# Kernel optimization log

Measured on AMD Instinct MI355X. Metric: run time of the kernel, lower is better.

Reference implementation:

```python
import jax, jax.numpy as jnp
import numpy as np

B, D, H, W = 32, 256, 32, 32
K = 1024
COMMITMENT_COST = 0.25


def setup_inputs() -> dict:
    key = jax.random.key(0)
    k1, k2 = jax.random.split(key)
    z = jax.random.normal(k1, (B, D, H, W), dtype=jnp.float32)
    # torch init: uniform_(-1/K, 1/K)
    emb_weight = jax.random.uniform(k2, (K, D), dtype=jnp.float32,
                                    minval=-1.0 / K, maxval=1.0 / K)
    return {"z": z, "emb_weight": emb_weight}


def reference(z, emb_weight):
    b, c, h, w = z.shape
    # [B, D, H, W] -> [B*H*W, D]
    z_flat = jnp.transpose(z, (0, 2, 3, 1)).reshape(-1, c)
    # squared-distance: ||z||^2 + ||e||^2 - 2 z.e  -> [N, K]
    distances = (jnp.sum(z_flat ** 2, axis=1, keepdims=True)
                 + jnp.sum(emb_weight ** 2, axis=1)[None, :]
                 - 2.0 * jnp.matmul(z_flat, emb_weight.T))
    encoding_indices = jnp.argmin(distances, axis=1)  # [N]
    z_q = emb_weight[encoding_indices]                # [N, D]
    z_q = z_q.reshape(b, h, w, c).transpose(0, 3, 1, 2)  # [B, D, H, W]

    q_latent_loss = jnp.mean((jax.lax.stop_gradient(z_q) - z) ** 2)
    e_latent_loss = jnp.mean((z_q - jax.lax.stop_gradient(z)) ** 2)
    loss = q_latent_loss + COMMITMENT_COST * e_latent_loss

    # straight-through estimator
    z_q = z + jax.lax.stop_gradient(z_q - z)
    return z_q, loss, encoding_indices
```

## Files before the change

kernel.cpp:

```cpp
#include <hip/hip_runtime.h>

#define NPTS  32768
#define DIM   256

#define ZQ_OFF   0
#define LOSS_OFF 8388608
#define IDX_OFF  8388609

typedef __attribute__((ext_vector_type(8))) short short8;
typedef __attribute__((ext_vector_type(4))) float f32x4;
typedef unsigned short ushort_t;
typedef unsigned int u32;
typedef unsigned long long u64;

__device__ __forceinline__ int z_base(int n) { return ((n >> 10) << 18) | (n & 1023); }

__device__ __forceinline__ ushort_t f2bf(float f) {
    u32 u = __float_as_uint(f);
    u += 0x7FFFu + ((u >> 16) & 1u);
    return (ushort_t)(u >> 16);
}

__device__ __forceinline__ u64 pack_vi(float v, int i) {
    u32 u = __float_as_uint(v);
    u32 key = (u & 0x80000000u) ? ~u : u;
    return ((u64)key << 32) | (u32)i;
}

__device__ __forceinline__ float np_half_sq(const float* __restrict__ p, int stride) {
    float S[16];
#pragma unroll
    for (int l = 0; l < 16; ++l) {
        float t[8];
#pragma unroll
        for (int j = 0; j < 8; ++j) {
            float v = p[(j * 16 + l) * stride];
            t[j] = __fmul_rn(v, v);
        }
        S[l] = __fadd_rn(__fadd_rn(__fadd_rn(t[0], t[1]), __fadd_rn(t[2], t[3])),
                         __fadd_rn(__fadd_rn(t[4], t[5]), __fadd_rn(t[6], t[7])));
    }
    float u[8];
#pragma unroll
    for (int i = 0; i < 8; ++i) u[i] = __fadd_rn(S[i], S[i + 8]);
    float v4[4];
#pragma unroll
    for (int i = 0; i < 4; ++i) v4[i] = __fadd_rn(u[i], u[i + 4]);
    return __fadd_rn(__fadd_rn(v4[0], v4[2]), __fadd_rn(v4[1], v4[3]));
}
__device__ __forceinline__ float np_sum256_sq(const float* __restrict__ p, int stride) {
    return __fadd_rn(np_half_sq(p, stride), np_half_sq(p + 128 * stride, stride));
}

__device__ __forceinline__ float np_half_sq_abs(const float* __restrict__ p, int stride, float* aacc) {
    float S[16]; float a = *aacc;
#pragma unroll
    for (int l = 0; l < 16; ++l) {
        float t[8];
#pragma unroll
        for (int j = 0; j < 8; ++j) {
            float v = p[(j * 16 + l) * stride];
            t[j] = __fmul_rn(v, v);
            a = __fadd_rn(a, fabsf(v));
        }
        S[l] = __fadd_rn(__fadd_rn(__fadd_rn(t[0], t[1]), __fadd_rn(t[2], t[3])),
                         __fadd_rn(__fadd_rn(t[4], t[5]), __fadd_rn(t[6], t[7])));
    }
    float u[8];
#pragma unroll
    for (int i = 0; i < 8; ++i) u[i] = __fadd_rn(S[i], S[i + 8]);
    float v4[4];
#pragma unroll
    for (int i = 0; i < 4; ++i) v4[i] = __fadd_rn(u[i], u[i + 4]);
    *aacc = a;
    return __fadd_rn(__fadd_rn(v4[0], v4[2]), __fadd_rn(v4[1], v4[3]));
}

__global__ __launch_bounds__(256) void setup_kernel(
    const float* __restrict__ z, const float* __restrict__ emb,
    float* __restrict__ z2, float* __restrict__ eps,
    float* __restrict__ e2, float* __restrict__ e2h,
    ushort_t* __restrict__ ebf, u64* __restrict__ bestG,
    double* __restrict__ loss_acc, unsigned int* __restrict__ ticket)
{
    if (blockIdx.x < 128) {
        int n = blockIdx.x * 256 + threadIdx.x;
        const float* p = z + z_base(n);
        float a = 0.0f;
        float h0 = np_half_sq_abs(p, 1024, &a);
        float h1 = np_half_sq_abs(p + 128 * 1024, 1024, &a);
        z2[n] = __fadd_rn(h0, h1);
        eps[n] = __builtin_fmaf(1e-5f, a, 3e-4f);
        bestG[n] = 0x7FFFFFFFFFFFFFFFULL;
        if (blockIdx.x == 0 && threadIdx.x == 0) { *loss_acc = 0.0; *ticket = 0u; }
    } else {
        int kb = (blockIdx.x - 128) * 64;
        for (int i = threadIdx.x; i < 2048; i += 256) {
            int klocal = i >> 5, c = i & 31;
            int k = kb + klocal;
            int dt = c >> 2, lq = c & 3;
            int kt = k >> 5, nt = (k >> 4) & 1, lr = k & 15;
            const float* e = emb + k * 256 + dt * 32 + lq * 8;
            short8 ov;
#pragma unroll
            for (int j = 0; j < 8; ++j) ov[j] = (short)f2bf(e[j]);
            int f = kt * 16 + nt * 8 + dt;
            *(short8*)(ebf + (f << 9) + ((lq << 4) + lr) * 8) = ov;
        }
        if (threadIdx.x < 64) {
            int k = kb + threadIdx.x;
            float s = np_sum256_sq(emb + k * DIM, 1);
            e2[k] = s;
            e2h[k] = 0.5f * s;
        }
    }
}

__global__ __launch_bounds__(256, 4) void dist_kernel(
    const float* __restrict__ z, const float* __restrict__ emb,
    const ushort_t* __restrict__ ebf,
    const float* __restrict__ z2w, const float* __restrict__ e2w,
    const float* __restrict__ e2hw, const float* __restrict__ epsw,
    u64* __restrict__ bestG)
{
    __shared__ __align__(16) float zx[32 * 68];
    __shared__ __align__(16) int cl[2048];
    __shared__ float e2hS[1024];
    __shared__ unsigned int cntS[64];
    __shared__ int ovfS;

    const int tid = threadIdx.x;
    const int w  = tid >> 6;
    const int l  = tid & 63;
    const int lq = l >> 4;
    const int lr = l & 15;
    const int n0 = blockIdx.x << 6;
    const int zb = z_base(n0);
    const int pbase = w << 4;

    if (tid < 64) cntS[tid] = 0u;
    if (tid == 0) ovfS = 0;
    for (int i = tid; i < 1024; i += 256) e2hS[i] = e2hw[i];

    short8 af[8];
    {
        const float* zp = z + zb + pbase + lr;
#pragma unroll
        for (int dt = 0; dt < 8; ++dt)
#pragma unroll
            for (int j = 0; j < 8; ++j)
                af[dt][j] = (short)f2bf(zp[((dt << 5) + (lq << 3) + j) << 10]);
    }

    float4 epsv = *(const float4*)(epsw + n0 + pbase + (lq << 2));
    float eps_r[4] = { epsv.x, epsv.y, epsv.z, epsv.w };
    float Mr[4] = { -3.4e38f, -3.4e38f, -3.4e38f, -3.4e38f };

    __syncthreads();

    const ushort_t* fb = ebf + (l << 3);
    short8 B[2][2];
    B[0][0] = *(const short8*)(fb + (0 << 9));
    B[0][1] = *(const short8*)(fb + (8 << 9));
    B[1][0] = *(const short8*)(fb + (1 << 9));
    B[1][1] = *(const short8*)(fb + (9 << 9));

    f32x4 acc[2];
#pragma unroll
    for (int nt = 0; nt < 2; ++nt) {
        float e = e2hS[(nt << 4) + lr];
        f32x4 iv = { -e, -e, -e, -e };
        acc[nt] = iv;
    }

#pragma unroll 1
    for (int kt = 0; kt < 32; ++kt) {
        const int kt1 = (kt < 31) ? kt + 1 : 0;
#pragma unroll
        for (int dt = 0; dt < 8; ++dt) {
            const int p = dt & 1;
            __builtin_amdgcn_s_setprio(1);
            acc[0] = __builtin_amdgcn_mfma_f32_16x16x32_bf16(af[dt], B[p][0], acc[0], 0, 0, 0);
            acc[1] = __builtin_amdgcn_mfma_f32_16x16x32_bf16(af[dt], B[p][1], acc[1], 0, 0, 0);
            __builtin_amdgcn_s_setprio(0);
            const int dtn = dt + 2;
            const int fk = (dtn < 8) ? kt : kt1;
            const int f0 = fk * 16 + (dtn & 7);
            B[p][0] = *(const short8*)(fb + (f0 << 9));
            B[p][1] = *(const short8*)(fb + ((f0 + 8) << 9));
        }
        {
            float mx[4], thr[4];
#pragma unroll
            for (int r = 0; r < 4; ++r) mx[r] = fmaxf(acc[0][r], acc[1][r]);
#pragma unroll
            for (int s = 1; s <= 8; s <<= 1)
#pragma unroll
                for (int r = 0; r < 4; ++r)
                    mx[r] = fmaxf(mx[r], __shfl_xor(mx[r], s, 64));
#pragma unroll
            for (int r = 0; r < 4; ++r) {
                Mr[r] = fmaxf(Mr[r], mx[r]);
                thr[r] = Mr[r] - eps_r[r];
            }
#pragma unroll
            for (int nt = 0; nt < 2; ++nt)
#pragma unroll
                for (int r = 0; r < 4; ++r) {
                    if (acc[nt][r] >= thr[r]) {
                        int pp = pbase + lq * 4 + r;
                        int kk = (kt << 5) + (nt << 4) + lr;
                        unsigned int pos = atomicAdd(&cntS[pp], 1u);
                        if (pos < 32u) cl[pp * 32 + pos] = kk;
                        else atomicMax(&ovfS, 1);
                    }
                }
        }
        if (kt < 31) {
#pragma unroll
            for (int nt = 0; nt < 2; ++nt) {
                float e = e2hS[(kt1 << 5) + (nt << 4) + lr];
                f32x4 iv = { -e, -e, -e, -e };
                acc[nt] = iv;
            }
        }
    }
    __syncthreads();

    const int pt = tid & 63;
    const int s0 = tid >> 6;
    unsigned int nc = cntS[pt]; if (nc > 32u) nc = 32u;
    bool  act[8]; int kE[8]; float accE[8];
#pragma unroll
    for (int j = 0; j < 8; ++j) {
        unsigned int s = (unsigned int)s0 + 4u * j;
        act[j] = s < nc;
        kE[j] = act[j] ? cl[pt * 32 + s] : 0;
        accE[j] = 0.0f;
    }
#pragma unroll 1
    for (int dt = 0; dt < 8; ++dt) {
        const int dbase = dt * 32;
        __syncthreads();
        {
            int q = tid & 15, dd0 = tid >> 4;
            float4 v0 = *(const float4*)(z + zb + ((dbase + dd0) << 10) + 4 * q);
            float4 v1 = *(const float4*)(z + zb + ((dbase + dd0 + 16) << 10) + 4 * q);
            *(float4*)(zx + dd0 * 68 + 4 * q) = v0;
            *(float4*)(zx + (dd0 + 16) * 68 + 4 * q) = v1;
        }
        __syncthreads();
#pragma unroll
        for (int j = 0; j < 8; ++j) {
            if (!act[j]) continue;
            const float* er = emb + kE[j] * 256 + dbase;
            float ev[32];
#pragma unroll
            for (int c = 0; c < 8; ++c) *(float4*)(ev + 4 * c) = *(const float4*)(er + 4 * c);
            float a = accE[j];
#pragma unroll
            for (int dd = 0; dd < 32; ++dd)
                a = __builtin_fmaf(zx[dd * 68 + pt], ev[dd], a);
            accE[j] = a;
        }
    }
#pragma unroll
    for (int j = 0; j < 8; ++j) {
        if (!act[j]) continue;
        int k = kE[j];
        float t1 = __fadd_rn(z2w[n0 + pt], e2w[k]);
        float d  = __fsub_rn(t1, __fmul_rn(2.0f, accE[j]));
        atomicMin(&bestG[n0 + pt], pack_vi(d, k));
    }
    __syncthreads();

    if (ovfS) {
        for (int row = 0; row < 64; ++row) {
            if (cntS[row] <= 32u) continue;
            float fa[4] = {0.f, 0.f, 0.f, 0.f};
            for (int dt = 0; dt < 8; ++dt) {
                const int dbase = dt * 32;
                __syncthreads();
                {
                    int q = tid & 15, dd0 = tid >> 4;
                    float4 v0 = *(const float4*)(z + zb + ((dbase + dd0) << 10) + 4 * q);
                    float4 v1 = *(const float4*)(z + zb + ((dbase + dd0 + 16) << 10) + 4 * q);
                    *(float4*)(zx + dd0 * 68 + 4 * q) = v0;
                    *(float4*)(zx + (dd0 + 16) * 68 + 4 * q) = v1;
                }
                __syncthreads();
                for (int c = 0; c < 4; ++c) {
                    const float* er = emb + (tid + 256 * c) * 256 + dbase;
                    for (int dd = 0; dd < 32; ++dd)
                        fa[c] = __builtin_fmaf(zx[dd * 68 + row], er[dd], fa[c]);
                }
            }
            for (int c = 0; c < 4; ++c) {
                int k = tid + 256 * c;
                float t1 = __fadd_rn(z2w[n0 + row], e2w[k]);
                float d  = __fsub_rn(t1, __fmul_rn(2.0f, fa[c]));
                atomicMin(&bestG[n0 + row], pack_vi(d, k));
            }
            __syncthreads();
        }
    }
}

__global__ __launch_bounds__(256) void zq_loss_kernel(
    const float* __restrict__ z, const float* __restrict__ emb,
    const u64* __restrict__ bestG, float* __restrict__ zq,
    double* __restrict__ loss_acc, unsigned int* __restrict__ ticket,
    float* __restrict__ out_loss, float* __restrict__ out_idx)
{
    const int tl = threadIdx.x & 63;
    const int q  = threadIdx.x >> 6;
    const int n  = blockIdx.x * 64 + tl;
    const int kk = (int)(u32)(bestG[n] & 0xFFFFFFFFULL);
    if (q == 0) out_idx[n] = (float)kk;
    const float4* er4 = (const float4*)(emb + kk * DIM + (q << 6));
    const int zb2 = z_base(n) + (q << 16);
    double s = 0.0;
#pragma unroll 4
    for (int c = 0; c < 16; ++c) {
        float4 e4 = er4[c];
#pragma unroll
        for (int j = 0; j < 4; ++j) {
            int dd = c * 4 + j;
            float ev = (j == 0) ? e4.x : (j == 1) ? e4.y : (j == 2) ? e4.z : e4.w;
            float zv = z[zb2 + (dd << 10)];
            zq[zb2 + (dd << 10)] = ev;
            float df = ev - zv;
            s = fma((double)df, (double)df, s);
        }
    }
    for (int off = 32; off; off >>= 1) s += __shfl_down(s, off, 64);
    __shared__ double sred[4];
    if ((threadIdx.x & 63) == 0) sred[threadIdx.x >> 6] = s;
    __syncthreads();
    if (threadIdx.x == 0) {
        atomicAdd(loss_acc, (sred[0] + sred[1]) + (sred[2] + sred[3]));
        __threadfence();
        unsigned int old = atomicAdd(ticket, 1u);
        if (old == gridDim.x - 1) {
            double total = atomicAdd(loss_acc, 0.0);
            out_loss[0] = (float)(1.25 * (total / 8388608.0));
        }
    }
}

extern "C" void kernel_launch(void* const* d_in, const int* in_sizes, int n_in,
                              void* d_out, int out_size, void* d_ws, size_t ws_size,
                              hipStream_t stream) {
    const float* z   = (const float*)d_in[0];
    const float* emb = (const float*)d_in[1];
    float* out = (float*)d_out;

    float* z2w = (float*)d_ws;
    float* epsw = (float*)((char*)d_ws + 131072);
    float* e2w = (float*)((char*)d_ws + 262144);
    float* e2hw = (float*)((char*)d_ws + 266240);
    ushort_t* ebf = (ushort_t*)((char*)d_ws + 270336);
    double* loss_acc = (double*)((char*)d_ws + 794624);
    unsigned int* ticket = (unsigned int*)((char*)d_ws + 794632);
    u64* bestG = (u64*)((char*)d_ws + 794640);

    setup_kernel<<<144, 256, 0, stream>>>(z, emb, z2w, epsw, e2w, e2hw, ebf,
                                          bestG, loss_acc, ticket);
    dist_kernel<<<NPTS / 64, 256, 0, stream>>>(z, emb, ebf, z2w, e2w, e2hw,
                                               epsw, bestG);
    zq_loss_kernel<<<NPTS / 64, 256, 0, stream>>>(z, emb, bestG, out + ZQ_OFF,
                                                  loss_acc, ticket,
                                                  out + LOSS_OFF, out + IDX_OFF);
}
```

Before: 218.1 us.

## Retile distance kernel to 2x2 MFMA tiles and split setup/zq work finer

```diff
diff --git a/kernel.cpp b/kernel.cpp
--- a/kernel.cpp
+++ b/kernel.cpp
@@ -83,18 +83,23 @@
     ushort_t* __restrict__ ebf, u64* __restrict__ bestG,
     double* __restrict__ loss_acc, unsigned int* __restrict__ ticket)
 {
-    if (blockIdx.x < 128) {
-        int n = blockIdx.x * 256 + threadIdx.x;
-        const float* p = z + z_base(n);
+    if (blockIdx.x < 256) {
+        __shared__ float hbuf[128], abuf[128];
+        const int tl = threadIdx.x & 127;
+        const int half = threadIdx.x >> 7;
+        const int n = blockIdx.x * 128 + tl;
+        const float* p = z + z_base(n) + (half << 17);
         float a = 0.0f;
-        float h0 = np_half_sq_abs(p, 1024, &a);
-        float h1 = np_half_sq_abs(p + 128 * 1024, 1024, &a);
-        z2[n] = __fadd_rn(h0, h1);
-        eps[n] = __builtin_fmaf(1e-5f, a, 3e-4f);
-        bestG[n] = 0x7FFFFFFFFFFFFFFFULL;
+        float hs = np_half_sq_abs(p, 1024, &a);
+        if (half) { hbuf[tl] = hs; abuf[tl] = a; bestG[n] = 0x7FFFFFFFFFFFFFFFULL; }
+        __syncthreads();
+        if (!half) {
+            z2[n] = __fadd_rn(hs, hbuf[tl]);
+            eps[n] = __builtin_fmaf(1e-5f, a + abuf[tl], 3e-4f);
+        }
         if (blockIdx.x == 0 && threadIdx.x == 0) { *loss_acc = 0.0; *ticket = 0u; }
     } else {
-        int kb = (blockIdx.x - 128) * 64;
+        int kb = (blockIdx.x - 256) * 64;
         for (int i = threadIdx.x; i < 2048; i += 256) {
             int klocal = i >> 5, c = i & 31;
             int k = kb + klocal;
@@ -116,7 +121,7 @@
     }
 }
 
-__global__ __launch_bounds__(256, 4) void dist_kernel(
+__global__ __launch_bounds__(256, 2) void dist_kernel(
     const float* __restrict__ z, const float* __restrict__ emb,
     const ushort_t* __restrict__ ebf,
     const float* __restrict__ z2w, const float* __restrict__ e2w,
@@ -131,97 +136,119 @@
 
     const int tid = threadIdx.x;
     const int w  = tid >> 6;
+    const int ph = w & 1;
+    const int kh = w >> 1;
     const int l  = tid & 63;
     const int lq = l >> 4;
     const int lr = l & 15;
     const int n0 = blockIdx.x << 6;
     const int zb = z_base(n0);
-    const int pbase = w << 4;
+    const int pbase = ph << 5;
 
     if (tid < 64) cntS[tid] = 0u;
     if (tid == 0) ovfS = 0;
     for (int i = tid; i < 1024; i += 256) e2hS[i] = e2hw[i];
 
-    short8 af[8];
-    {
-        const float* zp = z + zb + pbase + lr;
+    short8 af[2][8];
+#pragma unroll
+    for (int mt = 0; mt < 2; ++mt) {
+        const float* zp = z + zb + pbase + (mt << 4) + lr;
 #pragma unroll
         for (int dt = 0; dt < 8; ++dt)
 #pragma unroll
             for (int j = 0; j < 8; ++j)
-                af[dt][j] = (short)f2bf(zp[((dt << 5) + (lq << 3) + j) << 10]);
-    }
-
-    float4 epsv = *(const float4*)(epsw + n0 + pbase + (lq << 2));
-    float eps_r[4] = { epsv.x, epsv.y, epsv.z, epsv.w };
-    float Mr[4] = { -3.4e38f, -3.4e38f, -3.4e38f, -3.4e38f };
+                af[mt][dt][j] = (short)f2bf(zp[((dt << 5) + (lq << 3) + j) << 10]);
+    }
+
+    float eps_r[2][4], Mr[2][4];
+#pragma unroll
+    for (int mt = 0; mt < 2; ++mt) {
+        float4 ev = *(const float4*)(epsw + n0 + pbase + (mt << 4) + (lq << 2));
+        eps_r[mt][0] = ev.x; eps_r[mt][1] = ev.y; eps_r[mt][2] = ev.z; eps_r[mt][3] = ev.w;
+#pragma unroll
+        for (int r = 0; r < 4; ++r) Mr[mt][r] = -3.4e38f;
+    }
 
     __syncthreads();
 
     const ushort_t* fb = ebf + (l << 3);
-    short8 B[2][2];
-    B[0][0] = *(const short8*)(fb + (0 << 9));
-    B[0][1] = *(const short8*)(fb + (8 << 9));
-    B[1][0] = *(const short8*)(fb + (1 << 9));
-    B[1][1] = *(const short8*)(fb + (9 << 9));
-
-    f32x4 acc[2];
+    const int ktg0 = kh << 4;
+    short8 B[4][2];
+#pragma unroll
+    for (int i = 0; i < 4; ++i) {
+        const int f0 = (ktg0 << 4) + i;
+        B[i][0] = *(const short8*)(fb + (f0 << 9));
+        B[i][1] = *(const short8*)(fb + ((f0 + 8) << 9));
+    }
+
+    f32x4 acc[2][2];
 #pragma unroll
     for (int nt = 0; nt < 2; ++nt) {
-        float e = e2hS[(nt << 4) + lr];
+        float e = e2hS[(ktg0 << 5) + (nt << 4) + lr];
         f32x4 iv = { -e, -e, -e, -e };
-        acc[nt] = iv;
+        acc[0][nt] = iv; acc[1][nt] = iv;
     }
 
 #pragma unroll 1
-    for (int kt = 0; kt < 32; ++kt) {
-        const int kt1 = (kt < 31) ? kt + 1 : 0;
+    for (int kt = 0; kt < 16; ++kt) {
+        const int ktg = ktg0 + kt;
 #pragma unroll
         for (int dt = 0; dt < 8; ++dt) {
-            const int p = dt & 1;
+            const int p = dt & 3;
             __builtin_amdgcn_s_setprio(1);
-            acc[0] = __builtin_amdgcn_mfma_f32_16x16x32_bf16(af[dt], B[p][0], acc[0], 0, 0, 0);
-            acc[1] = __builtin_amdgcn_mfma_f32_16x16x32_bf16(af[dt], B[p][1], acc[1], 0, 0, 0);
+            acc[0][0] = __builtin_amdgcn_mfma_f32_16x16x32_bf16(af[0][dt], B[p][0], acc[0][0], 0, 0, 0);
+            acc[0][1] = __builtin_amdgcn_mfma_f32_16x16x32_bf16(af[0][dt], B[p][1], acc[0][1], 0, 0, 0);
+            acc[1][0] = __builtin_amdgcn_mfma_f32_16x16x32_bf16(af[1][dt], B[p][0], acc[1][0], 0, 0, 0);
+            acc[1][1] = __builtin_amdgcn_mfma_f32_16x16x32_bf16(af[1][dt], B[p][1], acc[1][1], 0, 0, 0);
             __builtin_amdgcn_s_setprio(0);
-            const int dtn = dt + 2;
-            const int fk = (dtn < 8) ? kt : kt1;
-            const int f0 = fk * 16 + (dtn & 7);
-            B[p][0] = *(const short8*)(fb + (f0 << 9));
-            B[p][1] = *(const short8*)(fb + ((f0 + 8) << 9));
+            const int ndt = (dt + 4) & 7;
+            const int nktg = (dt >= 4) ? ((ktg + 1) & 31) : ktg;
+            const int nf0 = (nktg << 4) + ndt;
+            B[p][0] = *(const short8*)(fb + (nf0 << 9));
+            B[p][1] = *(const short8*)(fb + ((nf0 + 8) << 9));
         }
         {
-            float mx[4], thr[4];
-#pragma unroll
-            for (int r = 0; r < 4; ++r) mx[r] = fmaxf(acc[0][r], acc[1][r]);
+            float mx[2][4], thr[2][4];
+#pragma unroll
+            for (int mt = 0; mt < 2; ++mt)
+#pragma unroll
+                for (int r = 0; r < 4; ++r)
+                    mx[mt][r] = fmaxf(acc[mt][0][r], acc[mt][1][r]);
 #pragma unroll
             for (int s = 1; s <= 8; s <<= 1)
 #pragma unroll
-                for (int r = 0; r < 4; ++r)
-                    mx[r] = fmaxf(mx[r], __shfl_xor(mx[r], s, 64));
-#pragma unroll
-            for (int r = 0; r < 4; ++r) {
-                Mr[r] = fmaxf(Mr[r], mx[r]);
-                thr[r] = Mr[r] - eps_r[r];
-            }
-#pragma unroll
-            for (int nt = 0; nt < 2; ++nt)
+                for (int mt = 0; mt < 2; ++mt)
+#pragma unroll
+                    for (int r = 0; r < 4; ++r)
+                        mx[mt][r] = fmaxf(mx[mt][r], __shfl_xor(mx[mt][r], s, 64));
+#pragma unroll
+            for (int mt = 0; mt < 2; ++mt)
 #pragma unroll
                 for (int r = 0; r < 4; ++r) {
-                    if (acc[nt][r] >= thr[r]) {
-                        int pp = pbase + lq * 4 + r;
-                        int kk = (kt << 5) + (nt << 4) + lr;
-                        unsigned int pos = atomicAdd(&cntS[pp], 1u);
-                        if (pos < 32u) cl[pp * 32 + pos] = kk;
-                        else atomicMax(&ovfS, 1);
+                    Mr[mt][r] = fmaxf(Mr[mt][r], mx[mt][r]);
+                    thr[mt][r] = Mr[mt][r] - eps_r[mt][r];
+                }
+#pragma unroll
+            for (int mt = 0; mt < 2; ++mt)
+#pragma unroll
+                for (int nt = 0; nt < 2; ++nt)
+#pragma unroll
+                    for (int r = 0; r < 4; ++r) {
+                        if (acc[mt][nt][r] >= thr[mt][r]) {
+                            int pp = pbase + (mt << 4) + lq * 4 + r;
+                            int kk = (ktg << 5) + (nt << 4) + lr;
+                            unsigned int pos = atomicAdd(&cntS[pp], 1u);
+                            if (pos < 32u) cl[pp * 32 + pos] = kk;
+                            else atomicMax(&ovfS, 1);
+                        }
                     }
-                }
-        }
-        if (kt < 31) {
+        }
+        if (kt < 15) {
 #pragma unroll
             for (int nt = 0; nt < 2; ++nt) {
-                float e = e2hS[(kt1 << 5) + (nt << 4) + lr];
+                float e = e2hS[((ktg + 1) << 5) + (nt << 4) + lr];
                 f32x4 iv = { -e, -e, -e, -e };
-                acc[nt] = iv;
+                acc[0][nt] = iv; acc[1][nt] = iv;
             }
         }
     }
@@ -312,16 +339,16 @@
     double* __restrict__ loss_acc, unsigned int* __restrict__ ticket,
     float* __restrict__ out_loss, float* __restrict__ out_idx)
 {
-    const int tl = threadIdx.x & 63;
-    const int q  = threadIdx.x >> 6;
-    const int n  = blockIdx.x * 64 + tl;
+    const int tl = threadIdx.x & 31;
+    const int sl = threadIdx.x >> 5;
+    const int n  = blockIdx.x * 32 + tl;
     const int kk = (int)(u32)(bestG[n] & 0xFFFFFFFFULL);
-    if (q == 0) out_idx[n] = (float)kk;
-    const float4* er4 = (const float4*)(emb + kk * DIM + (q << 6));
-    const int zb2 = z_base(n) + (q << 16);
+    if (sl == 0) out_idx[n] = (float)kk;
+    const float4* er4 = (const float4*)(emb + kk * DIM + (sl << 5));
+    const int zb2 = z_base(n) + (sl << 15);
     double s = 0.0;
-#pragma unroll 4
-    for (int c = 0; c < 16; ++c) {
+#pragma unroll
+    for (int c = 0; c < 8; ++c) {
         float4 e4 = er4[c];
 #pragma unroll
         for (int j = 0; j < 4; ++j) {
@@ -364,11 +391,11 @@
     unsigned int* ticket = (unsigned int*)((char*)d_ws + 794632);
     u64* bestG = (u64*)((char*)d_ws + 794640);
 
-    setup_kernel<<<144, 256, 0, stream>>>(z, emb, z2w, epsw, e2w, e2hw, ebf,
+    setup_kernel<<<272, 256, 0, stream>>>(z, emb, z2w, epsw, e2w, e2hw, ebf,
                                           bestG, loss_acc, ticket);
     dist_kernel<<<NPTS / 64, 256, 0, stream>>>(z, emb, ebf, z2w, e2w, e2hw,
                                                epsw, bestG);
-    zq_loss_kernel<<<NPTS / 64, 256, 0, stream>>>(z, emb, bestG, out + ZQ_OFF,
+    zq_loss_kernel<<<NPTS / 32, 256, 0, stream>>>(z, emb, bestG, out + ZQ_OFF,
                                                   loss_acc, ticket,
                                                   out + LOSS_OFF, out + IDX_OFF);
 }
```

Result: slower. 283.5 us (+30.0%).
